# Kernel optimization log

Measured on AMD Instinct MI355X. Metric: run time of the kernel, lower is better.

The kernel has to match this reference:

```python
import jax, jax.numpy as jnp
import numpy as np

B, T, H = 64, 1024, 256

def _lstm_cell(x, h, c, Wih, Whh, bih, bhh):
    # torch gate order: i, f, g, o
    gates = x @ Wih.T + h @ Whh.T + bih + bhh  # [B, 4H]
    i, f, g, o = jnp.split(gates, 4, axis=-1)
    i = jax.nn.sigmoid(i)
    f = jax.nn.sigmoid(f)
    g = jnp.tanh(g)
    o = jax.nn.sigmoid(o)
    c_new = f * c + i * g
    h_new = o * jnp.tanh(c_new)
    return h_new, c_new


def setup_inputs() -> dict:
    key = jax.random.key(0)
    ks = jax.random.split(key, 11)
    s = 1.0 / np.sqrt(H)
    def u(k, shape):
        return jax.random.uniform(k, shape, jnp.float32, -s, s)
    return {
        "x": jax.random.normal(ks[0], (B, T, 1), jnp.float32),
        "enc_Wih": u(ks[1], (4 * H, 1)),
        "enc_Whh": u(ks[2], (4 * H, H)),
        "enc_bih": u(ks[3], (4 * H,)),
        "enc_bhh": u(ks[4], (4 * H,)),
        "dec_Wih": u(ks[5], (4 * H, 1)),
        "dec_Whh": u(ks[6], (4 * H, H)),
        "dec_bih": u(ks[7], (4 * H,)),
        "dec_bhh": u(ks[8], (4 * H,)),
        "lin_W": u(ks[9], (1, 2 * H)),
        "lin_b": u(ks[10], (1,)),
    }


def reference(x, enc_Wih, enc_Whh, enc_bih, enc_bhh,
              dec_Wih, dec_Whh, dec_bih, dec_bhh, lin_W, lin_b):
    b = x.shape[0]
    h = x.shape[2] * 0  # placeholder, not used
    hidden = enc_Whh.shape[1]

    x_t = jnp.transpose(x, (1, 0, 2))  # [T, B, 1]

    # ---- encoder: single-layer LSTM over time ----
    def enc_step(carry, xt):
        hh, cc = carry
        hh, cc = _lstm_cell(xt, hh, cc, enc_Wih, enc_Whh, enc_bih, enc_bhh)
        return (hh, cc), hh
    h0 = jnp.zeros((b, hidden), x.dtype)
    (h_last, _), enc_seq = jax.lax.scan(enc_step, (h0, h0), x_t)
    encoder_states = jnp.transpose(enc_seq, (1, 0, 2))  # [B, T, H]

    # ---- decoder: LSTMCell + dot attention + linear, per step ----
    def dec_step(carry, xt):
        hx, cx = carry
        hx, cx = _lstm_cell(xt, hx, cx, dec_Wih, dec_Whh, dec_bih, dec_bhh)
        scores = jnp.einsum('bth,bh->bt', encoder_states, hx)  # dot attention
        attn = jax.nn.softmax(scores, axis=1)
        ctx = jnp.einsum('bt,bth->bh', attn, encoder_states)
        updated = jnp.concatenate([ctx, hx], axis=1)  # [B, 2H]
        res = updated @ lin_W.T + lin_b  # [B, 1]
        return (hx, cx), res

    cx0 = jnp.zeros_like(h_last)
    _, outs = jax.lax.scan(dec_step, (h_last, cx0), x_t)  # [T, B, 1]
    return jnp.transpose(outs, (1, 0, 2))  # [B, T, 1]
```

## Files before the change

kernel.cpp:

```cpp
#include <hip/hip_runtime.h>
#include <math.h>

#define HD 256
#define GD 1024
#define TT 1024
#define BB 64
#define NT 512
#define PROBE_SPINS 5000
#define STEP_SPINS  3000

__device__ __forceinline__ float sig_(float x)  { return 1.f / (1.f + __expf(-x)); }
__device__ __forceinline__ float tanh_(float x) { return 1.f - 2.f / (1.f + __expf(2.f * x)); }

__global__ __launch_bounds__(256) void prep_kernel(
    const float* __restrict__ eW, const float* __restrict__ eb1, const float* __restrict__ eb2,
    const float* __restrict__ dW, const float* __restrict__ db1, const float* __restrict__ db2,
    float* __restrict__ WTe, float* __restrict__ WTd,
    float* __restrict__ be, float* __restrict__ bd,
    unsigned long long* __restrict__ ex_all,
    unsigned* __restrict__ probe_all)
{
    int idx = blockIdx.x * 256 + threadIdx.x;
    if (idx < GD * HD) {
        int j = idx / HD, k = idx % HD;
        WTe[k * GD + j] = eW[idx];
        WTd[k * GD + j] = dW[idx];
    }
    if (idx < GD) {
        be[idx] = eb1[idx] + eb2[idx];
        bd[idx] = db1[idx] + db2[idx];
    }
    if (idx < 2 * BB * 2 * 256) ex_all[idx] = 0ULL;
    if (idx < 1024) probe_all[idx] = 0u;
}

__global__ __launch_bounds__(NT, 2) void lstm_scan_coop(
    const float* __restrict__ x,
    const float* __restrict__ Wih,
    const float* __restrict__ bias,
    const float* __restrict__ WT,
    const float* __restrict__ h_init,
    float* __restrict__ states,
    unsigned long long* __restrict__ ex_fast,
    unsigned long long* __restrict__ ex_slow,
    unsigned* __restrict__ pf,
    unsigned* __restrict__ okv,
    unsigned tag0)
{
    const int b   = blockIdx.x & 63;
    const int q   = blockIdx.x >> 6;
    const int tid = threadIdx.x;
    const int s   = tid & 3;
    const int jj  = tid >> 2;
    const int gate = jj >> 5;
    const int kk0  = (jj & 31) * 2;
    const int r0   = gate * 64 + kk0;
    const int jg0  = gate * 256 + q * 64 + kk0;

    __shared__ float h_rep[4][264];
    __shared__ float act_s[256];
    __shared__ float x_s[TT];
    __shared__ int fast_sh;

    if (tid == 0) {
        unsigned pv = 0xA5000000u | (unsigned)(q + 1);
        unsigned* fp = pf + b * 4 + q;
        asm volatile("global_store_dword %0, %1, off" :: "v"(fp), "v"(pv) : "memory");
        int okall = 1;
        #pragma unroll 1
        for (int i = 0; i < 4; ++i) {
            if (i == q) continue;
            const unsigned* pp = pf + b * 4 + i;
            const unsigned expect = 0xA5000000u | (unsigned)(i + 1);
            int got = 0;
            #pragma unroll 1
            for (int it = 0; it < PROBE_SPINS; ++it) {
                unsigned u;
                asm volatile("global_load_dword %0, %1, off sc0\n\ts_waitcnt vmcnt(0)"
                             : "=&v"(u) : "v"(pp) : "memory");
                if (u == expect) { got = 1; break; }
            }
            okall &= got;
        }
        __hip_atomic_store(&okv[b * 4 + q], 0x100u | (unsigned)okall,
                           __ATOMIC_RELAXED, __HIP_MEMORY_SCOPE_AGENT);
        int f = 1;
        #pragma unroll 1
        for (int i = 0; i < 4; ++i) {
            unsigned u;
            do {
                u = __hip_atomic_load(&okv[b * 4 + i], __ATOMIC_RELAXED, __HIP_MEMORY_SCOPE_AGENT);
            } while (!(u & 0x100u));
            f &= (int)(u & 1u);
        }
        fast_sh = f;
    }

    float4 w0[16], w1[16];
    {
        const float* basek = WT + (size_t)(s * 64) * GD;
        #pragma unroll
        for (int i = 0; i < 16; ++i) {
            const float* p0 = basek + (size_t)(4 * i) * GD + jg0;
            w0[i] = make_float4(p0[0], p0[GD], p0[2 * GD], p0[3 * GD]);
            const float* p1 = p0 + 1;
            w1[i] = make_float4(p1[0], p1[GD], p1[2 * GD], p1[3 * GD]);
        }
    }
    const float wih0 = Wih[jg0], wih1 = Wih[jg0 + 1];
    const float bj0  = bias[jg0], bj1  = bias[jg0 + 1];

    for (int i = tid; i < TT; i += NT) x_s[i] = x[b * TT + i];
    if (tid < 256) {
        float hv = h_init ? h_init[((size_t)b * TT + (TT - 1)) * HD + tid] : 0.f;
        h_rep[tid >> 6][tid & 63] = hv;
    }
    float c = 0.f;
    __syncthreads();

    for (int t = 0; t < TT; ++t) {
        const float xt = x_s[t];
        float a0p, a1p, a0q = 0.f, a1q = 0.f;
        if (s == 0) { a0p = fmaf(xt, wih0, bj0); a1p = fmaf(xt, wih1, bj1); }
        else        { a0p = 0.f;                 a1p = 0.f; }
        const float4* h4 = (const float4*)(&h_rep[s][0]);
        #pragma unroll
        for (int i = 0; i < 8; ++i) {
            float4 hv = h4[i];
            a0p = fmaf(hv.x, w0[i].x, a0p); a0p = fmaf(hv.y, w0[i].y, a0p);
            a0p = fmaf(hv.z, w0[i].z, a0p); a0p = fmaf(hv.w, w0[i].w, a0p);
            a1p = fmaf(hv.x, w1[i].x, a1p); a1p = fmaf(hv.y, w1[i].y, a1p);
            a1p = fmaf(hv.z, w1[i].z, a1p); a1p = fmaf(hv.w, w1[i].w, a1p);
        }
        #pragma unroll
        for (int i = 8; i < 16; ++i) {
            float4 hv = h4[i];
            a0q = fmaf(hv.x, w0[i].x, a0q); a0q = fmaf(hv.y, w0[i].y, a0q);
            a0q = fmaf(hv.z, w0[i].z, a0q); a0q = fmaf(hv.w, w0[i].w, a0q);
            a1q = fmaf(hv.x, w1[i].x, a1q); a1q = fmaf(hv.y, w1[i].y, a1q);
            a1q = fmaf(hv.z, w1[i].z, a1q); a1q = fmaf(hv.w, w1[i].w, a1q);
        }
        float a0 = a0p + a0q;
        float a1 = a1p + a1q;
        a0 += __shfl_xor(a0, 1); a0 += __shfl_xor(a0, 2);
        a1 += __shfl_xor(a1, 1); a1 += __shfl_xor(a1, 2);
        if (s == 0) {
            float2 av;
            av.x = (gate == 2) ? tanh_(a0) : sig_(a0);
            av.y = (gate == 2) ? tanh_(a1) : sig_(a1);
            *(float2*)(&act_s[r0]) = av;
        }
        __syncthreads();

        const unsigned tag = tag0 + (unsigned)t + 1u;
        unsigned long long* fsl = ex_fast + ((size_t)b * 2 + (t & 1)) * 256;
        unsigned long long* ssl = ex_slow + ((size_t)b * 2 + (t & 1)) * 256;
        if (tid < 256) {
            const int dq = tid >> 6, dk = tid & 63;
            if (dq == q) {
                float gi = act_s[dk], gf = act_s[64 + dk], gg = act_s[128 + dk], go = act_s[192 + dk];
                c = fmaf(gf, c, gi * gg);
                float h = go * tanh_(c);
                unsigned long long pk = ((unsigned long long)tag << 32)
                                      | (unsigned long long)__float_as_uint(h);
                {
                    unsigned long long* fp2 = fsl + tid;
                    asm volatile("global_store_dwordx2 %0, %1, off"
                                 :: "v"(fp2), "v"(pk) : "memory");
                }
                __hip_atomic_store(&ssl[tid], pk, __ATOMIC_RELAXED, __HIP_MEMORY_SCOPE_AGENT);
                h_rep[q][dk] = h;
                states[((size_t)(b * TT + t)) * HD + tid] = h;
            } else {
                unsigned long long u;
                int got = 0;
                if (fast_sh) {
                    const unsigned long long* fp2 = fsl + tid;
                    #pragma unroll 1
                    for (int it = 0; it < STEP_SPINS; ++it) {
                        asm volatile("global_load_dwordx2 %0, %1, off sc0\n\ts_waitcnt vmcnt(0)"
                                     : "=&v"(u) : "v"(fp2) : "memory");
                        if ((unsigned)(u >> 32) == tag) { got = 1; break; }
                    }
                    if (!got) fast_sh = 0;
                }
                if (!got) {
                    do {
                        u = __hip_atomic_load(&ssl[tid], __ATOMIC_RELAXED, __HIP_MEMORY_SCOPE_AGENT);
                    } while ((unsigned)(u >> 32) != tag);
                }
                h_rep[dq][dk] = __uint_as_float((unsigned)u);
            }
        }
        __syncthreads();
    }
}

__global__ __launch_bounds__(256) void proj_kernel(
    const float* __restrict__ enc_states, const float* __restrict__ dec_hs,
    const float* __restrict__ linW, float* __restrict__ ew, float* __restrict__ hw)
{
    const int lane = threadIdx.x & 63;
    const int wid  = blockIdx.x * 4 + (threadIdx.x >> 6);
    const int nw   = gridDim.x * 4;
    const float4 w1 = ((const float4*)linW)[lane];
    const float4 w2 = ((const float4*)(linW + HD))[lane];
    for (int o = wid; o < BB * TT; o += nw) {
        float4 v1 = ((const float4*)(enc_states + (size_t)o * HD))[lane];
        float4 v2 = ((const float4*)(dec_hs     + (size_t)o * HD))[lane];
        float s1 = v1.x * w1.x + v1.y * w1.y + v1.z * w1.z + v1.w * w1.w;
        float s2 = v2.x * w2.x + v2.y * w2.y + v2.z * w2.z + v2.w * w2.w;
        #pragma unroll
        for (int m = 1; m < 64; m <<= 1) {
            s1 += __shfl_xor(s1, m);
            s2 += __shfl_xor(s2, m);
        }
        if (lane == 0) { ew[o] = s1; hw[o] = s2; }
    }
}

#define TD2  32
#define TEC2 256
#define KC2  32
__global__ __launch_bounds__(256) void attn_kernel(
    const float* __restrict__ enc_states,
    const float* __restrict__ dec_hs,
    const float* __restrict__ ew, const float* __restrict__ hw,
    const float* __restrict__ lin_b,
    float* __restrict__ out)
{
    const int b   = blockIdx.y;
    const int td0 = blockIdx.x * TD2;
    const int tid = threadIdx.x;
    const int tdt = tid >> 5;
    const int tet = tid & 31;

    __shared__ float Hx[HD][TD2 + 4];
    __shared__ float E[KC2][TEC2];

    {
        const int td = tid >> 3;
        const int kc = (tid & 7) * 32;
        const float* src = dec_hs + ((size_t)b * TT + td0 + td) * HD + kc;
        #pragma unroll
        for (int qq = 0; qq < 8; ++qq) {
            float4 v = ((const float4*)(src + qq * 4))[0];
            Hx[kc + qq * 4 + 0][td] = v.x;
            Hx[kc + qq * 4 + 1][td] = v.y;
            Hx[kc + qq * 4 + 2][td] = v.z;
            Hx[kc + qq * 4 + 3][td] = v.w;
        }
    }

    float M[4]  = {-1e30f, -1e30f, -1e30f, -1e30f};
    float Nm[4] = {0.f, 0.f, 0.f, 0.f};
    float Dn[4] = {0.f, 0.f, 0.f, 0.f};

    for (int tc = 0; tc < TT / TEC2; ++tc) {
        const int te0 = tc * TEC2;
        float S[4][8] = {{0.f}};
        for (int kc = 0; kc < HD / KC2; ++kc) {
            const int k0 = kc * KC2;
            __syncthreads();
            {
                const float* src = enc_states + ((size_t)b * TT + te0 + tid) * HD + k0;
                #pragma unroll
                for (int qq = 0; qq < 8; ++qq) {
                    float4 v = ((const float4*)(src + qq * 4))[0];
                    E[qq * 4 + 0][tid] = v.x;
                    E[qq * 4 + 1][tid] = v.y;
                    E[qq * 4 + 2][tid] = v.z;
                    E[qq * 4 + 3][tid] = v.w;
                }
            }
            __syncthreads();
            #pragma unroll 4
            for (int k = 0; k < KC2; ++k) {
                const float4 hx4 = *(const float4*)(&Hx[k0 + k][tdt * 4]);
                #pragma unroll
                for (int i = 0; i < 8; ++i) {
                    const float e = E[k][tet + 32 * i];
                    S[0][i] = fmaf(hx4.x, e, S[0][i]);
                    S[1][i] = fmaf(hx4.y, e, S[1][i]);
                    S[2][i] = fmaf(hx4.z, e, S[2][i]);
                    S[3][i] = fmaf(hx4.w, e, S[3][i]);
                }
            }
        }
        float ewv[8];
        #pragma unroll
        for (int i = 0; i < 8; ++i) ewv[i] = ew[(size_t)b * TT + te0 + tet + 32 * i];
        #pragma unroll
        for (int r = 0; r < 4; ++r) {
            float cm = S[r][0];
            #pragma unroll
            for (int i = 1; i < 8; ++i) cm = fmaxf(cm, S[r][i]);
            #pragma unroll
            for (int m = 1; m < 32; m <<= 1) cm = fmaxf(cm, __shfl_xor(cm, m));
            const float newM  = fmaxf(M[r], cm);
            const float scale = __expf(M[r] - newM);
            float nl = 0.f, dl = 0.f;
            #pragma unroll
            for (int i = 0; i < 8; ++i) {
                const float p = __expf(S[r][i] - newM);
                dl += p;
                nl = fmaf(p, ewv[i], nl);
            }
            #pragma unroll
            for (int m = 1; m < 32; m <<= 1) {
                nl += __shfl_xor(nl, m);
                dl += __shfl_xor(dl, m);
            }
            Nm[r] = Nm[r] * scale + nl;
            Dn[r] = Dn[r] * scale + dl;
            M[r]  = newM;
        }
    }

    if (tet == 0) {
        const float lb = lin_b[0];
        #pragma unroll
        for (int r = 0; r < 4; ++r) {
            const int td = td0 + tdt * 4 + r;
            out[(size_t)b * TT + td] = Nm[r] / Dn[r] + hw[(size_t)b * TT + td] + lb;
        }
    }
}

extern "C" void kernel_launch(void* const* d_in, const int* in_sizes, int n_in,
                              void* d_out, int out_size, void* d_ws, size_t ws_size,
                              hipStream_t stream)
{
    const float* x    = (const float*)d_in[0];
    const float* eWih = (const float*)d_in[1];
    const float* eWhh = (const float*)d_in[2];
    const float* ebih = (const float*)d_in[3];
    const float* ebhh = (const float*)d_in[4];
    const float* dWih = (const float*)d_in[5];
    const float* dWhh = (const float*)d_in[6];
    const float* dbih = (const float*)d_in[7];
    const float* dbhh = (const float*)d_in[8];
    const float* linW = (const float*)d_in[9];
    const float* linb = (const float*)d_in[10];
    float* out = (float*)d_out;

    float* p = (float*)d_ws;
    float* WTe = p;        p += (size_t)GD * HD;
    float* WTd = p;        p += (size_t)GD * HD;
    float* be  = p;        p += GD;
    float* bd  = p;        p += GD;
    float* enc_states = p; p += (size_t)BB * TT * HD;
    float* dec_hs = p;     p += (size_t)BB * TT * HD;
    float* ew = p;         p += (size_t)BB * TT;
    float* hw = p;         p += (size_t)BB * TT;
    unsigned long long* ex_fast = (unsigned long long*)p; p += (size_t)BB * 2 * 256 * 2;
    unsigned long long* ex_slow = (unsigned long long*)p; p += (size_t)BB * 2 * 256 * 2;
    unsigned* pf_e = (unsigned*)out;
    unsigned* pf_d = pf_e + 256;
    unsigned* ok_e = pf_e + 512;
    unsigned* ok_d = pf_e + 768;

    prep_kernel<<<(GD * HD + 255) / 256, 256, 0, stream>>>(
        eWhh, ebih, ebhh, dWhh, dbih, dbhh, WTe, WTd, be, bd,
        ex_fast, (unsigned*)out);

    unsigned tag0e = 0u, tag0d = 1024u;
    {
        const float* hi = nullptr;
        void* args[] = {(void*)&x, (void*)&eWih, (void*)&be, (void*)&WTe,
                        (void*)&hi, (void*)&enc_states, (void*)&ex_fast,
                        (void*)&ex_slow, (void*)&pf_e, (void*)&ok_e, (void*)&tag0e};
        hipLaunchCooperativeKernel((void*)lstm_scan_coop, dim3(256), dim3(NT),
                                   args, 0, stream);
    }
    {
        const float* hi = enc_states;
        void* args[] = {(void*)&x, (void*)&dWih, (void*)&bd, (void*)&WTd,
                        (void*)&hi, (void*)&dec_hs, (void*)&ex_fast,
                        (void*)&ex_slow, (void*)&pf_d, (void*)&ok_d, (void*)&tag0d};
        hipLaunchCooperativeKernel((void*)lstm_scan_coop, dim3(256), dim3(NT),
                                   args, 0, stream);
    }

    proj_kernel<<<256, 256, 0, stream>>>(enc_states, dec_hs, linW, ew, hw);
    attn_kernel<<<dim3(TT / TD2, BB), 256, 0, stream>>>(enc_states, dec_hs, ew, hw, linb, out);
}
```

Before: 4.320 ms.

## Launch LSTM scans normally, parallelize co-residency probe, chunk decoder block mapping

Replaces the cooperative launches with ordinary kernel launches. The four partner blocks of each batch are now probed in parallel by four lanes and combined with a ballot. The decoder maps each batch's four blocks to adjacent block IDs, and the probe and step spin limits are lowered so a slow fallback is detected sooner. This aims to cut launch overhead and startup probe latency. It relies on the runtime probe and slow-path fallback for correctness, since co-residency is no longer guaranteed. The pf/ok scratch offsets are also rearranged.

```diff
diff --git a/kernel.cpp b/kernel.cpp
--- a/kernel.cpp
+++ b/kernel.cpp
@@ -6,8 +6,8 @@
 #define TT 1024
 #define BB 64
 #define NT 512
-#define PROBE_SPINS 5000
-#define STEP_SPINS  3000
+#define PROBE_SPINS 600
+#define STEP_SPINS  1200
 
 __device__ __forceinline__ float sig_(float x)  { return 1.f / (1.f + __expf(-x)); }
 __device__ __forceinline__ float tanh_(float x) { return 1.f - 2.f / (1.f + __expf(2.f * x)); }
@@ -45,10 +45,11 @@
     unsigned long long* __restrict__ ex_slow,
     unsigned* __restrict__ pf,
     unsigned* __restrict__ okv,
-    unsigned tag0)
-{
-    const int b   = blockIdx.x & 63;
-    const int q   = blockIdx.x >> 6;
+    unsigned tag0,
+    int chunked)
+{
+    const int b   = chunked ? ((int)blockIdx.x >> 2) : ((int)blockIdx.x & 63);
+    const int q   = chunked ? ((int)blockIdx.x & 3)  : ((int)blockIdx.x >> 6);
     const int tid = threadIdx.x;
     const int s   = tid & 3;
     const int jj  = tid >> 2;
@@ -62,38 +63,41 @@
     __shared__ float x_s[TT];
     __shared__ int fast_sh;
 
-    if (tid == 0) {
-        unsigned pv = 0xA5000000u | (unsigned)(q + 1);
-        unsigned* fp = pf + b * 4 + q;
-        asm volatile("global_store_dword %0, %1, off" :: "v"(fp), "v"(pv) : "memory");
-        int okall = 1;
-        #pragma unroll 1
-        for (int i = 0; i < 4; ++i) {
-            if (i == q) continue;
-            const unsigned* pp = pf + b * 4 + i;
-            const unsigned expect = 0xA5000000u | (unsigned)(i + 1);
-            int got = 0;
+    if (tid < 4) {
+        if (tid == q) {
+            unsigned* fp = pf + b * 4 + q;
+            unsigned pv = 0xA5000000u | (unsigned)(q + 1);
+            asm volatile("global_store_dword %0, %1, off" :: "v"(fp), "v"(pv) : "memory");
+        }
+        int ok = 1;
+        if (tid != q) {
+            const unsigned* pp = pf + b * 4 + tid;
+            const unsigned expect = 0xA5000000u | (unsigned)(tid + 1);
+            ok = 0;
             #pragma unroll 1
             for (int it = 0; it < PROBE_SPINS; ++it) {
                 unsigned u;
                 asm volatile("global_load_dword %0, %1, off sc0\n\ts_waitcnt vmcnt(0)"
                              : "=&v"(u) : "v"(pp) : "memory");
-                if (u == expect) { got = 1; break; }
-            }
-            okall &= got;
-        }
-        __hip_atomic_store(&okv[b * 4 + q], 0x100u | (unsigned)okall,
-                           __ATOMIC_RELAXED, __HIP_MEMORY_SCOPE_AGENT);
-        int f = 1;
-        #pragma unroll 1
-        for (int i = 0; i < 4; ++i) {
-            unsigned u;
-            do {
-                u = __hip_atomic_load(&okv[b * 4 + i], __ATOMIC_RELAXED, __HIP_MEMORY_SCOPE_AGENT);
-            } while (!(u & 0x100u));
-            f &= (int)(u & 1u);
-        }
-        fast_sh = f;
+                if (u == expect) { ok = 1; break; }
+            }
+        }
+        unsigned long long m = __ballot(ok != 0);
+        if (tid == 0) {
+            int okall = ((m & 0xFull) == 0xFull) ? 1 : 0;
+            __hip_atomic_store(&okv[b * 4 + q], 0x100u | (unsigned)okall,
+                               __ATOMIC_RELAXED, __HIP_MEMORY_SCOPE_AGENT);
+            int f = 1;
+            #pragma unroll 1
+            for (int i = 0; i < 4; ++i) {
+                unsigned u;
+                do {
+                    u = __hip_atomic_load(&okv[b * 4 + i], __ATOMIC_RELAXED, __HIP_MEMORY_SCOPE_AGENT);
+                } while (!(u & 0x100u));
+                f &= (int)(u & 1u);
+            }
+            fast_sh = f;
+        }
     }
 
     float4 w0[16], w1[16];
@@ -356,31 +360,20 @@
     unsigned long long* ex_fast = (unsigned long long*)p; p += (size_t)BB * 2 * 256 * 2;
     unsigned long long* ex_slow = (unsigned long long*)p; p += (size_t)BB * 2 * 256 * 2;
     unsigned* pf_e = (unsigned*)out;
-    unsigned* pf_d = pf_e + 256;
-    unsigned* ok_e = pf_e + 512;
+    unsigned* ok_e = pf_e + 256;
+    unsigned* pf_d = pf_e + 512;
     unsigned* ok_d = pf_e + 768;
 
     prep_kernel<<<(GD * HD + 255) / 256, 256, 0, stream>>>(
         eWhh, ebih, ebhh, dWhh, dbih, dbhh, WTe, WTd, be, bd,
         ex_fast, (unsigned*)out);
 
-    unsigned tag0e = 0u, tag0d = 1024u;
-    {
-        const float* hi = nullptr;
-        void* args[] = {(void*)&x, (void*)&eWih, (void*)&be, (void*)&WTe,
-                        (void*)&hi, (void*)&enc_states, (void*)&ex_fast,
-                        (void*)&ex_slow, (void*)&pf_e, (void*)&ok_e, (void*)&tag0e};
-        hipLaunchCooperativeKernel((void*)lstm_scan_coop, dim3(256), dim3(NT),
-                                   args, 0, stream);
-    }
-    {
-        const float* hi = enc_states;
-        void* args[] = {(void*)&x, (void*)&dWih, (void*)&bd, (void*)&WTd,
-                        (void*)&hi, (void*)&dec_hs, (void*)&ex_fast,
-                        (void*)&ex_slow, (void*)&pf_d, (void*)&ok_d, (void*)&tag0d};
-        hipLaunchCooperativeKernel((void*)lstm_scan_coop, dim3(256), dim3(NT),
-                                   args, 0, stream);
-    }
+    lstm_scan_coop<<<256, NT, 0, stream>>>(
+        x, eWih, be, WTe, nullptr, enc_states,
+        ex_fast, ex_slow, pf_e, ok_e, 0u, 0);
+    lstm_scan_coop<<<256, NT, 0, stream>>>(
+        x, dWih, bd, WTd, enc_states, dec_hs,
+        ex_fast, ex_slow, pf_d, ok_d, 1024u, 1);
 
     proj_kernel<<<256, 256, 0, stream>>>(enc_states, dec_hs, linW, ew, hw);
     attn_kernel<<<dim3(TT / TD2, BB), 256, 0, stream>>>(enc_states, dec_hs, ew, hw, linb, out);
```

Result: faster. 4.082 ms (-5.5%).
